# Optimization experiments

Measured on AMD Instinct MI355X. Metric: run time of the kernel, lower is better.

Reference implementation:

```python
import jax, jax.numpy as jnp
import numpy as np

HID = 16  # module-level output_size constant
D = 64    # input_dim
K = 32    # number of classes / outer nets
B = 8192  # batch


def setup_inputs() -> dict:
    key = jax.random.key(0)
    ks = jax.random.split(key, 9)
    s = 0.1
    return {
        "x": jax.random.normal(ks[0], (B, D), dtype=jnp.float32),
        # inner nets: one tiny 1->16->1 MLP per (k, i)
        "iw1": jax.random.normal(ks[1], (K, D, HID), dtype=jnp.float32) * s,  # Linear(1,16) weight
        "ib1": jax.random.normal(ks[2], (K, D, HID), dtype=jnp.float32) * s,  # Linear(1,16) bias
        "iw2": jax.random.normal(ks[3], (K, D, HID), dtype=jnp.float32) * s,  # Linear(16,1) weight
        "ib2": jax.random.normal(ks[4], (K, D), dtype=jnp.float32) * s,       # Linear(16,1) bias
        # outer nets: one 1->16->1 MLP per k
        "ow1": jax.random.normal(ks[5], (K, HID), dtype=jnp.float32) * s,
        "ob1": jax.random.normal(ks[6], (K, HID), dtype=jnp.float32) * s,
        "ow2": jax.random.normal(ks[7], (K, HID), dtype=jnp.float32) * s,
        "ob2": jax.random.normal(ks[8], (K,), dtype=jnp.float32) * s,
    }


def reference(x, iw1, ib1, iw2, ib2, ow1, ob1, ow2, ob2):
    # Inner nets, all K*D at once. Linear(1,HID) on scalar xi is an outer product.
    # h: [B, K, D, HID]
    h = jax.nn.relu(x[:, None, :, None] * iw1[None] + ib1[None])
    # Linear(HID,1): contract HID -> yi: [B, K, D]
    yi = jnp.einsum('bkdh,kdh->bkd', h, iw2) + ib2[None]
    # sum over input features i -> [B, K]
    sk = yi.sum(axis=2)
    # Outer nets: scalar -> HID -> scalar per k
    g = jax.nn.relu(sk[:, :, None] * ow1[None] + ob1[None])  # [B, K, HID]
    out = jnp.einsum('bkh,kh->bk', g, ow2) + ob2[None]       # [B, K]
    return out
```

## Files before the change

### kernel.cpp

```cpp
#include <hip/hip_runtime.h>
#include <hip/hip_bf16.h>

#define HID 16
#define DIN 64
#define NK  32
#define NB  8192

typedef float v2f __attribute__((ext_vector_type(2)));
typedef float v4f __attribute__((ext_vector_type(4)));

__global__ __launch_bounds__(256, 4) void kan_kernel(
    const float* __restrict__ x,
    const float* __restrict__ iw1, const float* __restrict__ ib1,
    const float* __restrict__ iw2, const float* __restrict__ ib2,
    const float* __restrict__ ow1, const float* __restrict__ ob1,
    const float* __restrict__ ow2, const float* __restrict__ ob2,
    float* __restrict__ out)
{
    const int k = blockIdx.x & (NK - 1);
    const int b = (blockIdx.x >> 5) * 256 + threadIdx.x;

    const v2f* __restrict__ w1p = (const v2f*)(iw1 + k * DIN * HID);
    const v2f* __restrict__ b1p = (const v2f*)(ib1 + k * DIN * HID);
    const v2f* __restrict__ w2p = (const v2f*)(iw2 + k * DIN * HID);
    const float* __restrict__ c2k = ib2 + k * DIN;

    const float* __restrict__ xr = x + b * DIN;

    v2f acc[4];
    acc[0] = acc[1] = acc[2] = acc[3] = (v2f){0.f, 0.f};
    float bsum = 0.f;

    for (int d0 = 0; d0 < DIN; d0 += 4) {
        const v4f xv = *(const v4f*)(xr + d0);
        #pragma unroll
        for (int dd = 0; dd < 4; ++dd) {
            const int d = d0 + dd;
            const float xd = xv[dd];
            const v2f xx = {xd, xd};
            #pragma unroll
            for (int hp = 0; hp < 8; ++hp) {
                const v2f w1 = w1p[d * 8 + hp];
                const v2f bb = b1p[d * 8 + hp];
                const v2f w2 = w2p[d * 8 + hp];
                v2f t = __builtin_elementwise_fma(xx, w1, bb);
                t = __builtin_elementwise_max(t, (v2f){0.f, 0.f});
                acc[hp & 3] = __builtin_elementwise_fma(t, w2, acc[hp & 3]);
            }
            bsum += c2k[d];
        }
    }

    const float sk = acc[0].x + acc[0].y + acc[1].x + acc[1].y
                   + acc[2].x + acc[2].y + acc[3].x + acc[3].y + bsum;

    float o = ob2[k];
    #pragma unroll
    for (int h = 0; h < HID; ++h) {
        const float g = fmaxf(fmaf(sk, ow1[k * HID + h], ob1[k * HID + h]), 0.f);
        o = fmaf(g, ow2[k * HID + h], o);
    }

    out[b * NK + k] = o;
}

extern "C" void kernel_launch(void* const* d_in, const int* in_sizes, int n_in,
                              void* d_out, int out_size, void* d_ws, size_t ws_size,
                              hipStream_t stream) {
    const float* x   = (const float*)d_in[0];
    const float* iw1 = (const float*)d_in[1];
    const float* ib1 = (const float*)d_in[2];
    const float* iw2 = (const float*)d_in[3];
    const float* ib2 = (const float*)d_in[4];
    const float* ow1 = (const float*)d_in[5];
    const float* ob1 = (const float*)d_in[6];
    const float* ow2 = (const float*)d_in[7];
    const float* ob2 = (const float*)d_in[8];
    float* out = (float*)d_out;

    const int grid = (NB / 256) * NK;
    kan_kernel<<<grid, 256, 0, stream>>>(x, iw1, ib1, iw2, ib2,
                                         ow1, ob1, ow2, ob2, out);
}
```

Before: 31.01 us.

## Split input dimension across two thread halves with shared-memory reduction

Each block now covers 128 batch rows, and its two 128-thread halves each process half of the 64 input features for the same row. Partial sums are combined through shared memory before the outer MLP, and the grid doubles. The launch bound occupancy hint rises from 4 to 8. The aim is more parallelism and shorter per-thread dependency chains, at the cost of a barrier, half the threads idling in the epilogue, and tighter register limits.

```diff
diff --git a/kernel.cpp b/kernel.cpp
--- a/kernel.cpp
+++ b/kernel.cpp
@@ -9,7 +9,7 @@
 typedef float v2f __attribute__((ext_vector_type(2)));
 typedef float v4f __attribute__((ext_vector_type(4)));
 
-__global__ __launch_bounds__(256, 4) void kan_kernel(
+__global__ __launch_bounds__(256, 8) void kan_kernel(
     const float* __restrict__ x,
     const float* __restrict__ iw1, const float* __restrict__ ib1,
     const float* __restrict__ iw2, const float* __restrict__ ib2,
@@ -17,21 +17,28 @@
     const float* __restrict__ ow2, const float* __restrict__ ob2,
     float* __restrict__ out)
 {
-    const int k = blockIdx.x & (NK - 1);
-    const int b = (blockIdx.x >> 5) * 256 + threadIdx.x;
+    __shared__ float part[256];
 
-    const v2f* __restrict__ w1p = (const v2f*)(iw1 + k * DIN * HID);
-    const v2f* __restrict__ b1p = (const v2f*)(ib1 + k * DIN * HID);
-    const v2f* __restrict__ w2p = (const v2f*)(iw2 + k * DIN * HID);
-    const float* __restrict__ c2k = ib2 + k * DIN;
+    const int k     = blockIdx.x & (NK - 1);
+    const int chunk = blockIdx.x >> 5;
+    const int t     = threadIdx.x;
+    const int bl    = t & 127;
+    const int dh    = __builtin_amdgcn_readfirstlane(t >> 7);
+    const int b     = chunk * 128 + bl;
+    const int dbase = dh * 32;
 
-    const float* __restrict__ xr = x + b * DIN;
+    const v2f* __restrict__ w1p = (const v2f*)(iw1 + (k * DIN + dbase) * HID);
+    const v2f* __restrict__ b1p = (const v2f*)(ib1 + (k * DIN + dbase) * HID);
+    const v2f* __restrict__ w2p = (const v2f*)(iw2 + (k * DIN + dbase) * HID);
+    const float* __restrict__ c2k = ib2 + k * DIN + dbase;
+
+    const float* __restrict__ xr = x + b * DIN + dbase;
 
     v2f acc[4];
     acc[0] = acc[1] = acc[2] = acc[3] = (v2f){0.f, 0.f};
     float bsum = 0.f;
 
-    for (int d0 = 0; d0 < DIN; d0 += 4) {
+    for (int d0 = 0; d0 < 32; d0 += 4) {
         const v4f xv = *(const v4f*)(xr + d0);
         #pragma unroll
         for (int dd = 0; dd < 4; ++dd) {
@@ -43,25 +50,28 @@
                 const v2f w1 = w1p[d * 8 + hp];
                 const v2f bb = b1p[d * 8 + hp];
                 const v2f w2 = w2p[d * 8 + hp];
-                v2f t = __builtin_elementwise_fma(xx, w1, bb);
-                t = __builtin_elementwise_max(t, (v2f){0.f, 0.f});
-                acc[hp & 3] = __builtin_elementwise_fma(t, w2, acc[hp & 3]);
+                v2f tv = __builtin_elementwise_fma(xx, w1, bb);
+                tv = __builtin_elementwise_max(tv, (v2f){0.f, 0.f});
+                acc[hp & 3] = __builtin_elementwise_fma(tv, w2, acc[hp & 3]);
             }
             bsum += c2k[d];
         }
     }
 
-    const float sk = acc[0].x + acc[0].y + acc[1].x + acc[1].y
-                   + acc[2].x + acc[2].y + acc[3].x + acc[3].y + bsum;
+    part[t] = acc[0].x + acc[0].y + acc[1].x + acc[1].y
+            + acc[2].x + acc[2].y + acc[3].x + acc[3].y + bsum;
+    __syncthreads();
 
-    float o = ob2[k];
-    #pragma unroll
-    for (int h = 0; h < HID; ++h) {
-        const float g = fmaxf(fmaf(sk, ow1[k * HID + h], ob1[k * HID + h]), 0.f);
-        o = fmaf(g, ow2[k * HID + h], o);
+    if (t < 128) {
+        const float sk = part[t] + part[t + 128];
+        float o = ob2[k];
+        #pragma unroll
+        for (int h = 0; h < HID; ++h) {
+            const float g = fmaxf(fmaf(sk, ow1[k * HID + h], ob1[k * HID + h]), 0.f);
+            o = fmaf(g, ow2[k * HID + h], o);
+        }
+        out[b * NK + k] = o;
     }
-
-    out[b * NK + k] = o;
 }
 
 extern "C" void kernel_launch(void* const* d_in, const int* in_sizes, int n_in,
@@ -78,7 +88,7 @@
     const float* ob2 = (const float*)d_in[8];
     float* out = (float*)d_out;
 
-    const int grid = (NB / 256) * NK;
+    const int grid = (NB / 128) * NK;
     kan_kernel<<<grid, 256, 0, stream>>>(x, iw1, ib1, iw2, ib2,
                                          ow1, ob1, ow2, ob2, out);
 }
```

Result: faster. 30.13 us (-2.9%).

## Map lanes to input features with register-held weights and butterfly shuffle reduction

Applied to the files above, without the earlier changes.

Each lane now owns one input feature d and keeps that feature's 48 inner-net weights in registers instead of re-reading all weights per batch row. A wave handles 64 batch rows: each lane loads x[row, lane] coalesced and evaluates its feature's MLP. A recursive-halving xor-shuffle tree then sums over features, leaving each lane with one row's sum in bit-reversed order, and the output index is permuted to match. This removes the per-thread weight loads and the strided x row reads, but adds 63 cross-lane shuffles per wave and more register pressure.

```diff
diff --git a/kernel.cpp b/kernel.cpp
--- a/kernel.cpp
+++ b/kernel.cpp
@@ -9,6 +9,42 @@
 typedef float v2f __attribute__((ext_vector_type(2)));
 typedef float v4f __attribute__((ext_vector_type(4)));
 
+struct W {
+    v2f w1[8], b1[8], w2[8];
+};
+
+__device__ __forceinline__ float relu_dot(const W& w, float xd) {
+    const v2f xx = {xd, xd};
+    v2f acc0 = {0.f, 0.f}, acc1 = {0.f, 0.f};
+    #pragma unroll
+    for (int hp = 0; hp < 8; hp += 2) {
+        v2f t0 = __builtin_elementwise_fma(xx, w.w1[hp],     w.b1[hp]);
+        v2f t1 = __builtin_elementwise_fma(xx, w.w1[hp + 1], w.b1[hp + 1]);
+        t0 = __builtin_elementwise_max(t0, (v2f){0.f, 0.f});
+        t1 = __builtin_elementwise_max(t1, (v2f){0.f, 0.f});
+        acc0 = __builtin_elementwise_fma(t0, w.w2[hp],     acc0);
+        acc1 = __builtin_elementwise_fma(t1, w.w2[hp + 1], acc1);
+    }
+    const v2f a = acc0 + acc1;
+    return a.x + a.y;
+}
+
+template<int LVL, class F>
+__device__ __forceinline__ float subtree(int j0, int lane, const F& body) {
+    if constexpr (LVL == 0) {
+        return body(j0);
+    } else {
+        const float A = subtree<LVL - 1>(j0, lane, body);
+        const float B = subtree<LVL - 1>(j0 + (1 << (LVL - 1)), lane, body);
+        const int m = 64 >> LVL;
+        const bool hi = (lane & m) != 0;
+        const float send = hi ? A : B;
+        const float recv = __shfl_xor(send, m, 64);
+        const float keep = hi ? B : A;
+        return keep + recv;
+    }
+}
+
 __global__ __launch_bounds__(256, 4) void kan_kernel(
     const float* __restrict__ x,
     const float* __restrict__ iw1, const float* __restrict__ ib1,
@@ -17,42 +53,34 @@
     const float* __restrict__ ow2, const float* __restrict__ ob2,
     float* __restrict__ out)
 {
-    const int k = blockIdx.x & (NK - 1);
-    const int b = (blockIdx.x >> 5) * 256 + threadIdx.x;
+    const int k     = blockIdx.x & (NK - 1);
+    const int chunk = blockIdx.x >> 5;
+    const int t     = threadIdx.x;
+    const int lane  = t & 63;
+    const int wid   = t >> 6;
+    const int base  = chunk * 256 + wid * 64;
 
-    const v2f* __restrict__ w1p = (const v2f*)(iw1 + k * DIN * HID);
-    const v2f* __restrict__ b1p = (const v2f*)(ib1 + k * DIN * HID);
-    const v2f* __restrict__ w2p = (const v2f*)(iw2 + k * DIN * HID);
-    const float* __restrict__ c2k = ib2 + k * DIN;
-
-    const float* __restrict__ xr = x + b * DIN;
-
-    v2f acc[4];
-    acc[0] = acc[1] = acc[2] = acc[3] = (v2f){0.f, 0.f};
-    float bsum = 0.f;
-
-    for (int d0 = 0; d0 < DIN; d0 += 4) {
-        const v4f xv = *(const v4f*)(xr + d0);
+    W w;
+    {
+        const v4f* p1 = (const v4f*)(iw1 + (k * DIN + lane) * HID);
+        const v4f* p2 = (const v4f*)(ib1 + (k * DIN + lane) * HID);
+        const v4f* p3 = (const v4f*)(iw2 + (k * DIN + lane) * HID);
         #pragma unroll
-        for (int dd = 0; dd < 4; ++dd) {
-            const int d = d0 + dd;
-            const float xd = xv[dd];
-            const v2f xx = {xd, xd};
-            #pragma unroll
-            for (int hp = 0; hp < 8; ++hp) {
-                const v2f w1 = w1p[d * 8 + hp];
-                const v2f bb = b1p[d * 8 + hp];
-                const v2f w2 = w2p[d * 8 + hp];
-                v2f t = __builtin_elementwise_fma(xx, w1, bb);
-                t = __builtin_elementwise_max(t, (v2f){0.f, 0.f});
-                acc[hp & 3] = __builtin_elementwise_fma(t, w2, acc[hp & 3]);
-            }
-            bsum += c2k[d];
+        for (int q = 0; q < 4; ++q) {
+            ((v4f*)w.w1)[q] = p1[q];
+            ((v4f*)w.b1)[q] = p2[q];
+            ((v4f*)w.w2)[q] = p3[q];
         }
     }
 
-    const float sk = acc[0].x + acc[0].y + acc[1].x + acc[1].y
-                   + acc[2].x + acc[2].y + acc[3].x + acc[3].y + bsum;
+    float ck = ib2[k * DIN + lane];
+    #pragma unroll
+    for (int m = 32; m; m >>= 1) ck += __shfl_xor(ck, m, 64);
+
+    const float* __restrict__ xp = x + base * DIN + lane;
+    auto body = [&](int j) { return relu_dot(w, xp[j * DIN]); };
+
+    const float sk = subtree<6>(0, lane, body) + ck;
 
     float o = ob2[k];
     #pragma unroll
@@ -61,7 +89,8 @@
         o = fmaf(g, ow2[k * HID + h], o);
     }
 
-    out[b * NK + k] = o;
+    const int brev = (int)(__builtin_bitreverse32((unsigned)lane) >> 26);
+    out[(base + brev) * NK + k] = o;
 }
 
 extern "C" void kernel_launch(void* const* d_in, const int* in_sizes, int n_in,
```

Result: slower. 32.22 us (+3.9%).

## Rewrite ReLU MLPs as abs-form with precomputed weight transforms

Applied to the files above, without the earlier changes.

Adds a prep kernel that rewrites each 1->16->1 ReLU MLP using relu(z)=0.5(z+|z|), folding the linear part into per-(k,d) constants A and B. The stored breakpoints b1/w1 and scaled weights 0.5*w2*|w1| go into a padded workspace. The main kernel then evaluates each hidden unit as an add, an abs and an fma, and preloads the full x row into registers. This aims to cut per-unit arithmetic, at the cost of an extra launch and possible loss of packed-FP32 issue.

```diff
diff --git a/kernel.cpp b/kernel.cpp
--- a/kernel.cpp
+++ b/kernel.cpp
@@ -6,62 +6,108 @@
 #define NK  32
 #define NB  8192
 
-typedef float v2f __attribute__((ext_vector_type(2)));
+#define WSTRIDE 36
+#define OUTER_OFF (NK * DIN * WSTRIDE)
+
 typedef float v4f __attribute__((ext_vector_type(4)));
 
-__global__ __launch_bounds__(256, 4) void kan_kernel(
-    const float* __restrict__ x,
+__global__ void prep_kernel(
     const float* __restrict__ iw1, const float* __restrict__ ib1,
     const float* __restrict__ iw2, const float* __restrict__ ib2,
     const float* __restrict__ ow1, const float* __restrict__ ob1,
     const float* __restrict__ ow2, const float* __restrict__ ob2,
+    float* __restrict__ ws)
+{
+    const int tid = blockIdx.x * 256 + threadIdx.x;
+    if (tid < NK * DIN) {
+        const float* w1p = iw1 + tid * HID;
+        const float* b1p = ib1 + tid * HID;
+        const float* w2p = iw2 + tid * HID;
+        float* o = ws + tid * WSTRIDE;
+        float A = 0.f, B = ib2[tid];
+        #pragma unroll
+        for (int h = 0; h < HID; ++h) {
+            const float w1 = w1p[h], b1 = b1p[h], w2 = w2p[h];
+            A = fmaf(0.5f * w2, w1, A);
+            B = fmaf(0.5f * w2, b1, B);
+            const float aw = fabsf(w1);
+            const bool ok = aw > 1e-20f;
+            o[h]       = ok ? b1 / w1 : 0.f;
+            o[16 + h]  = ok ? 0.5f * w2 * aw : 0.f;
+            if (!ok) B = fmaf(0.5f * w2, fabsf(b1), B);
+        }
+        o[32] = A; o[33] = B; o[34] = 0.f; o[35] = 0.f;
+    } else if (tid < NK * DIN + NK) {
+        const int k = tid - NK * DIN;
+        const float* w1p = ow1 + k * HID;
+        const float* b1p = ob1 + k * HID;
+        const float* w2p = ow2 + k * HID;
+        float* o = ws + OUTER_OFF + k * WSTRIDE;
+        float A = 0.f, B = ob2[k];
+        #pragma unroll
+        for (int h = 0; h < HID; ++h) {
+            const float w1 = w1p[h], b1 = b1p[h], w2 = w2p[h];
+            A = fmaf(0.5f * w2, w1, A);
+            B = fmaf(0.5f * w2, b1, B);
+            const float aw = fabsf(w1);
+            const bool ok = aw > 1e-20f;
+            o[h]       = ok ? b1 / w1 : 0.f;
+            o[16 + h]  = ok ? 0.5f * w2 * aw : 0.f;
+            if (!ok) B = fmaf(0.5f * w2, fabsf(b1), B);
+        }
+        o[32] = A; o[33] = B; o[34] = 0.f; o[35] = 0.f;
+    }
+}
+
+__global__ __launch_bounds__(256, 4) void kan_main(
+    const float* __restrict__ x,
+    const float* __restrict__ ws,
     float* __restrict__ out)
 {
-    const int k = blockIdx.x & (NK - 1);
-    const int b = (blockIdx.x >> 5) * 256 + threadIdx.x;
+    const int t    = threadIdx.x;
+    const int lane = t & 63;
+    const int wid  = t >> 6;
+    const int k    = blockIdx.x & (NK - 1);
+    const int row  = (blockIdx.x >> 5) * 256 + wid * 64 + lane;
 
-    const v2f* __restrict__ w1p = (const v2f*)(iw1 + k * DIN * HID);
-    const v2f* __restrict__ b1p = (const v2f*)(ib1 + k * DIN * HID);
-    const v2f* __restrict__ w2p = (const v2f*)(iw2 + k * DIN * HID);
-    const float* __restrict__ c2k = ib2 + k * DIN;
+    v4f xw[16];
+    const v4f* xr = (const v4f*)(x + row * DIN);
+    #pragma unroll
+    for (int q = 0; q < 16; ++q) xw[q] = xr[q];
 
-    const float* __restrict__ xr = x + b * DIN;
+    const float* __restrict__ wk = ws + (k * DIN) * WSTRIDE;
 
-    v2f acc[4];
-    acc[0] = acc[1] = acc[2] = acc[3] = (v2f){0.f, 0.f};
-    float bsum = 0.f;
+    float acc0 = 0.f, acc1 = 0.f;
 
-    for (int d0 = 0; d0 < DIN; d0 += 4) {
-        const v4f xv = *(const v4f*)(xr + d0);
+    #pragma unroll 2
+    for (int dq = 0; dq < 16; ++dq) {
         #pragma unroll
-        for (int dd = 0; dd < 4; ++dd) {
-            const int d = d0 + dd;
-            const float xd = xv[dd];
-            const v2f xx = {xd, xd};
+        for (int j = 0; j < 4; ++j) {
+            const int d = dq * 4 + j;
+            const float xv = xw[dq][j];
+            const float* __restrict__ wd = wk + d * WSTRIDE;
+            acc0 = fmaf(wd[32], xv, acc0);
+            acc1 += wd[33];
             #pragma unroll
-            for (int hp = 0; hp < 8; ++hp) {
-                const v2f w1 = w1p[d * 8 + hp];
-                const v2f bb = b1p[d * 8 + hp];
-                const v2f w2 = w2p[d * 8 + hp];
-                v2f t = __builtin_elementwise_fma(xx, w1, bb);
-                t = __builtin_elementwise_max(t, (v2f){0.f, 0.f});
-                acc[hp & 3] = __builtin_elementwise_fma(t, w2, acc[hp & 3]);
+            for (int h = 0; h < HID; h += 2) {
+                acc0 = fmaf(fabsf(xv + wd[h]),     wd[16 + h],     acc0);
+                acc1 = fmaf(fabsf(xv + wd[h + 1]), wd[16 + h + 1], acc1);
             }
-            bsum += c2k[d];
         }
     }
+    const float sk = acc0 + acc1;
 
-    const float sk = acc[0].x + acc[0].y + acc[1].x + acc[1].y
-                   + acc[2].x + acc[2].y + acc[3].x + acc[3].y + bsum;
+    const float* __restrict__ wo = ws + OUTER_OFF + k * WSTRIDE;
+    float oa = 0.f, ob = 0.f;
+    #pragma unroll
+    for (int h = 0; h < HID; h += 2) {
+        oa = fmaf(fabsf(sk + wo[h]),     wo[16 + h],     oa);
+        ob = fmaf(fabsf(sk + wo[h + 1]), wo[16 + h + 1], ob);
+    }
+    oa = fmaf(wo[32], sk, oa);
+    ob += wo[33];
 
-    float o = ob2[k];
-    #pragma unroll
-    for (int h = 0; h < HID; ++h) {
-        const float g = fmaxf(fmaf(sk, ow1[k * HID + h], ob1[k * HID + h]), 0.f);
-        o = fmaf(g, ow2[k * HID + h], o);
-    }
-
-    out[b * NK + k] = o;
+    out[row * NK + k] = oa + ob;
 }
 
 extern "C" void kernel_launch(void* const* d_in, const int* in_sizes, int n_in,
@@ -76,9 +122,10 @@
     const float* ob1 = (const float*)d_in[6];
     const float* ow2 = (const float*)d_in[7];
     const float* ob2 = (const float*)d_in[8];
+    float* ws  = (float*)d_ws;
     float* out = (float*)d_out;
 
+    prep_kernel<<<9, 256, 0, stream>>>(iw1, ib1, iw2, ib2, ow1, ob1, ow2, ob2, ws);
     const int grid = (NB / 256) * NK;
-    kan_kernel<<<grid, 256, 0, stream>>>(x, iw1, ib1, iw2, ib2,
-                                         ow1, ob1, ow2, ob2, out);
+    kan_main<<<grid, 256, 0, stream>>>(x, ws, out);
 }
```

Result: slower. 46.27 us (+49.2%).
